# Kernel tuning notes

Measured on AMD Instinct MI355X. Metric: run time of the kernel, lower is better.

The kernel has to match this reference:

```python
import jax, jax.numpy as jnp
import numpy as np


def setup_inputs() -> dict:
    key = jax.random.key(0)
    k1, k2 = jax.random.split(key)
    N, S, C, H, W = 8, 6, 4, 512, 512
    preds = jax.random.normal(k1, (N, S, C, H, W), dtype=jnp.float32)
    targets = jax.random.randint(k2, (N, S, H, W), 0, C, dtype=jnp.int64)
    return {"preds": preds, "targets": targets}


def reference(preds, targets):
    # preds: [N, S, C, H, W], targets: [N, S, H, W]
    # Original: per (target_idx, lat, lon) F.cross_entropy (mean over batch),
    # summed over all pixels and target indices.
    logp = jax.nn.log_softmax(preds, axis=2)              # [N, S, C, H, W]
    tgt = targets[:, :, None, :, :]                        # [N, S, 1, H, W]
    nll = -jnp.take_along_axis(logp, tgt, axis=2)[:, :, 0]  # [N, S, H, W]
    # mean over batch N per pixel, then sum over S, H, W
    return jnp.sum(jnp.mean(nll, axis=0))
```

## Files before the change

### kernel.cpp

```cpp
#include <hip/hip_runtime.h>


#define HW        (512 * 512)
#define QUADS     (HW / 4)
#define NS        48
#define NBLK      ((NS * QUADS) / 256)
#define INV_N     0.125f

typedef float vf4 __attribute__((ext_vector_type(4)));
typedef int   vi4 __attribute__((ext_vector_type(4)));

__device__ __forceinline__ float nll_one(float a, float b, float c, float d, int t) {
    float m = fmaxf(fmaxf(a, b), fmaxf(c, d));
    float s = __expf(a - m) + __expf(b - m) + __expf(c - m) + __expf(d - m);
    float lse = m + __logf(s);
    float xt = (t == 0) ? a : ((t == 1) ? b : ((t == 2) ? c : d));
    return lse - xt;
}

__global__ __launch_bounds__(256) void ce_partial(const float* __restrict__ preds,
                                                  const int* __restrict__ targets,
                                                  float* __restrict__ part) {
    const int g  = blockIdx.x * 256 + threadIdx.x;
    const int ns = g >> 16;
    const int q  = g & (QUADS - 1);

    const vf4* __restrict__ p4 = (const vf4*)preds;
    const vi4* __restrict__ t4 = (const vi4*)targets;

    const int base = (ns << 2) * QUADS + q;
    vf4 x0 = __builtin_nontemporal_load(p4 + base);
    vf4 x1 = __builtin_nontemporal_load(p4 + base + QUADS);
    vf4 x2 = __builtin_nontemporal_load(p4 + base + 2 * QUADS);
    vf4 x3 = __builtin_nontemporal_load(p4 + base + 3 * QUADS);
    vi4 t  = __builtin_nontemporal_load(t4 + ns * QUADS + q);

    float lsum = nll_one(x0.x, x1.x, x2.x, x3.x, t.x)
               + nll_one(x0.y, x1.y, x2.y, x3.y, t.y)
               + nll_one(x0.z, x1.z, x2.z, x3.z, t.z)
               + nll_one(x0.w, x1.w, x2.w, x3.w, t.w);

    #pragma unroll
    for (int off = 32; off > 0; off >>= 1)
        lsum += __shfl_down(lsum, off, 64);

    __shared__ float wsum[4];
    const int lane = threadIdx.x & 63;
    const int wave = threadIdx.x >> 6;
    if (lane == 0) wsum[wave] = lsum;
    __syncthreads();
    if (threadIdx.x == 0)
        part[blockIdx.x] = (wsum[0] + wsum[1] + wsum[2] + wsum[3]) * INV_N;
}

__global__ __launch_bounds__(256) void ce_final(const float* __restrict__ part,
                                                float* __restrict__ out) {
    float lsum = 0.0f;
    #pragma unroll
    for (int i = 0; i < NBLK / 256; ++i)
        lsum += part[i * 256 + threadIdx.x];

    #pragma unroll
    for (int off = 32; off > 0; off >>= 1)
        lsum += __shfl_down(lsum, off, 64);

    __shared__ float wsum[4];
    const int lane = threadIdx.x & 63;
    const int wave = threadIdx.x >> 6;
    if (lane == 0) wsum[wave] = lsum;
    __syncthreads();
    if (threadIdx.x == 0)
        out[0] = wsum[0] + wsum[1] + wsum[2] + wsum[3];
}

extern "C" void kernel_launch(void* const* d_in, const int* in_sizes, int n_in,
                              void* d_out, int out_size, void* d_ws, size_t ws_size,
                              hipStream_t stream) {
    const float* preds   = (const float*)d_in[0];
    const int*   targets = (const int*)d_in[1];
    float*       part    = (float*)d_ws;
    float*       out     = (float*)d_out;

    ce_partial<<<NBLK, 256, 0, stream>>>(preds, targets, part);
    ce_final<<<1, 256, 0, stream>>>(part, out);
}
```

Before: 280.1 us.

## Use persistent grid-stride blocks with double-buffered register prefetch

Replaces the one-quad-per-thread launch (12288 blocks) with 2048 blocks where each thread handles six quads, striding by 8 slices. Loads for the next quad are issued before computing the current one, so two sets of 80 bytes are in flight per thread. This cuts block launch and partial-sum overhead and shrinks the final reduction, at the cost of more registers and fewer resident waves hiding latency.

New measurement: 374.4 us. +33.7%, slower.

```diff
diff --git a/kernel.cpp b/kernel.cpp
--- a/kernel.cpp
+++ b/kernel.cpp
@@ -1,11 +1,17 @@
 #include <hip/hip_runtime.h>
 
 
-#define HW        (512 * 512)
-#define QUADS     (HW / 4)
-#define NS        48
-#define NBLK      ((NS * QUADS) / 256)
-#define INV_N     0.125f
+#define HW      (512 * 512)
+#define QUADS   (HW / 4)
+#define NS      48
+#define NQUAD   (NS * QUADS)
+#define TPB     256
+#define PBLK    2048
+#define STRIDE  (PBLK * TPB)
+#define ITERS   (NQUAD / STRIDE)
+#define PADV    (8 * 4 * QUADS)
+#define TADV    (8 * QUADS)
+#define INV_N   0.125f
 
 typedef float vf4 __attribute__((ext_vector_type(4)));
 typedef int   vi4 __attribute__((ext_vector_type(4)));
@@ -18,27 +24,55 @@
     return lse - xt;
 }
 
-__global__ __launch_bounds__(256) void ce_partial(const float* __restrict__ preds,
-                                                  const int* __restrict__ targets,
-                                                  float* __restrict__ part) {
-    const int g  = blockIdx.x * 256 + threadIdx.x;
-    const int ns = g >> 16;
-    const int q  = g & (QUADS - 1);
+__device__ __forceinline__ float quad_nll(vf4 x0, vf4 x1, vf4 x2, vf4 x3, vi4 t) {
+    return nll_one(x0.x, x1.x, x2.x, x3.x, t.x)
+         + nll_one(x0.y, x1.y, x2.y, x3.y, t.y)
+         + nll_one(x0.z, x1.z, x2.z, x3.z, t.z)
+         + nll_one(x0.w, x1.w, x2.w, x3.w, t.w);
+}
 
-    const vf4* __restrict__ p4 = (const vf4*)preds;
-    const vi4* __restrict__ t4 = (const vi4*)targets;
+__global__ __launch_bounds__(TPB, 8) void ce_partial(const float* __restrict__ preds,
+                                                     const int* __restrict__ targets,
+                                                     float* __restrict__ part) {
+    const int g0  = blockIdx.x * TPB + threadIdx.x;
+    const int ns0 = g0 >> 16;
+    const int q   = g0 & (QUADS - 1);
 
-    const int base = (ns << 2) * QUADS + q;
-    vf4 x0 = __builtin_nontemporal_load(p4 + base);
-    vf4 x1 = __builtin_nontemporal_load(p4 + base + QUADS);
-    vf4 x2 = __builtin_nontemporal_load(p4 + base + 2 * QUADS);
-    vf4 x3 = __builtin_nontemporal_load(p4 + base + 3 * QUADS);
-    vi4 t  = __builtin_nontemporal_load(t4 + ns * QUADS + q);
+    const vf4* __restrict__ p4 = (const vf4*)preds + (size_t)ns0 * (4 * QUADS) + q;
+    const vi4* __restrict__ t4 = (const vi4*)targets + (size_t)ns0 * QUADS + q;
 
-    float lsum = nll_one(x0.x, x1.x, x2.x, x3.x, t.x)
-               + nll_one(x0.y, x1.y, x2.y, x3.y, t.y)
-               + nll_one(x0.z, x1.z, x2.z, x3.z, t.z)
-               + nll_one(x0.w, x1.w, x2.w, x3.w, t.w);
+    vf4 a0 = __builtin_nontemporal_load(p4 + 0 * QUADS);
+    vf4 a1 = __builtin_nontemporal_load(p4 + 1 * QUADS);
+    vf4 a2 = __builtin_nontemporal_load(p4 + 2 * QUADS);
+    vf4 a3 = __builtin_nontemporal_load(p4 + 3 * QUADS);
+    vi4 at = __builtin_nontemporal_load(t4);
+
+    float lsum = 0.0f;
+
+    #pragma unroll
+    for (int i = 0; i < ITERS; i += 2) {
+        const vf4* pb = p4 + (size_t)(i + 1) * PADV;
+        const vi4* tb = t4 + (size_t)(i + 1) * TADV;
+        vf4 b0 = __builtin_nontemporal_load(pb + 0 * QUADS);
+        vf4 b1 = __builtin_nontemporal_load(pb + 1 * QUADS);
+        vf4 b2 = __builtin_nontemporal_load(pb + 2 * QUADS);
+        vf4 b3 = __builtin_nontemporal_load(pb + 3 * QUADS);
+        vi4 bt = __builtin_nontemporal_load(tb);
+
+        lsum += quad_nll(a0, a1, a2, a3, at);
+
+        if (i + 2 < ITERS) {
+            const vf4* pa = p4 + (size_t)(i + 2) * PADV;
+            const vi4* ta = t4 + (size_t)(i + 2) * TADV;
+            a0 = __builtin_nontemporal_load(pa + 0 * QUADS);
+            a1 = __builtin_nontemporal_load(pa + 1 * QUADS);
+            a2 = __builtin_nontemporal_load(pa + 2 * QUADS);
+            a3 = __builtin_nontemporal_load(pa + 3 * QUADS);
+            at = __builtin_nontemporal_load(ta);
+        }
+
+        lsum += quad_nll(b0, b1, b2, b3, bt);
+    }
 
     #pragma unroll
     for (int off = 32; off > 0; off >>= 1)
@@ -57,7 +91,7 @@
                                                 float* __restrict__ out) {
     float lsum = 0.0f;
     #pragma unroll
-    for (int i = 0; i < NBLK / 256; ++i)
+    for (int i = 0; i < PBLK / 256; ++i)
         lsum += part[i * 256 + threadIdx.x];
 
     #pragma unroll
@@ -81,6 +115,6 @@
     float*       part    = (float*)d_ws;
     float*       out     = (float*)d_out;
 
-    ce_partial<<<NBLK, 256, 0, stream>>>(preds, targets, part);
+    ce_partial<<<PBLK, TPB, 0, stream>>>(preds, targets, part);
     ce_final<<<1, 256, 0, stream>>>(part, out);
 }
```

## Use persistent blocks with double-buffered async global-to-LDS loads

Applied to the files above, without the earlier changes.

Replaces the one-quad-per-thread grid with 1024 blocks that loop over the data. Each iteration prefetches the next tile straight into a double-buffered LDS region using global_load_lds and computes on the current tile. The aim is to overlap memory traffic with compute and to cut block-launch and partial-sum overhead. In exchange it adds two block barriers per iteration and LDS round trips, and it keeps fewer independent loads in flight per CU.

New measurement: 306.4 us. 1.09x slower.

```diff
diff --git a/kernel.cpp b/kernel.cpp
--- a/kernel.cpp
+++ b/kernel.cpp
@@ -1,11 +1,16 @@
 #include <hip/hip_runtime.h>
 
 
-#define HW        (512 * 512)
-#define QUADS     (HW / 4)
-#define NS        48
-#define NBLK      ((NS * QUADS) / 256)
-#define INV_N     0.125f
+#define HW      (512 * 512)
+#define QUADS   (HW / 4)
+#define NS      48
+#define NQUAD   (NS * QUADS)
+#define TPB     256
+#define PBLK    1024
+#define ITERS   (NQUAD / (PBLK * TPB))
+#define INV_N   0.125f
+
+#define BUF_FLOATS 5120
 
 typedef float vf4 __attribute__((ext_vector_type(4)));
 typedef int   vi4 __attribute__((ext_vector_type(4)));
@@ -18,38 +23,72 @@
     return lse - xt;
 }
 
-__global__ __launch_bounds__(256) void ce_partial(const float* __restrict__ preds,
+__device__ __forceinline__ float quad_nll(vf4 x0, vf4 x1, vf4 x2, vf4 x3, vi4 t) {
+    return nll_one(x0.x, x1.x, x2.x, x3.x, t.x)
+         + nll_one(x0.y, x1.y, x2.y, x3.y, t.y)
+         + nll_one(x0.z, x1.z, x2.z, x3.z, t.z)
+         + nll_one(x0.w, x1.w, x2.w, x3.w, t.w);
+}
+
+static __device__ __forceinline__ void gld16(const void* g, void* l) {
+    __builtin_amdgcn_global_load_lds(
+        (const __attribute__((address_space(1))) unsigned int*)g,
+        (__attribute__((address_space(3))) unsigned int*)l,
+        16, 0, 0);
+}
+
+__global__ __launch_bounds__(TPB) void ce_partial(const float* __restrict__ preds,
                                                   const int* __restrict__ targets,
                                                   float* __restrict__ part) {
-    const int g  = blockIdx.x * 256 + threadIdx.x;
-    const int ns = g >> 16;
-    const int q  = g & (QUADS - 1);
+    __shared__ float S[2 * BUF_FLOATS];
+
+    const int t    = threadIdx.x;
+    const int lane = t & 63;
+    const int wave = t >> 6;
 
     const vf4* __restrict__ p4 = (const vf4*)preds;
     const vi4* __restrict__ t4 = (const vi4*)targets;
 
-    const int base = (ns << 2) * QUADS + q;
-    vf4 x0 = __builtin_nontemporal_load(p4 + base);
-    vf4 x1 = __builtin_nontemporal_load(p4 + base + QUADS);
-    vf4 x2 = __builtin_nontemporal_load(p4 + base + 2 * QUADS);
-    vf4 x3 = __builtin_nontemporal_load(p4 + base + 3 * QUADS);
-    vi4 t  = __builtin_nontemporal_load(t4 + ns * QUADS + q);
+    float lsum = 0.0f;
 
-    float lsum = nll_one(x0.x, x1.x, x2.x, x3.x, t.x)
-               + nll_one(x0.y, x1.y, x2.y, x3.y, t.y)
-               + nll_one(x0.z, x1.z, x2.z, x3.z, t.z)
-               + nll_one(x0.w, x1.w, x2.w, x3.w, t.w);
+    auto stage = [&](int bb, int it) {
+        const int g0 = (it * PBLK + (int)blockIdx.x) * TPB;
+        const int ns = g0 >> 16;
+        const int q0 = g0 & (QUADS - 1);
+        const int qq = q0 + wave * 64 + lane;
+        float* dst = &S[bb * BUF_FLOATS + wave * 256];
+        #pragma unroll
+        for (int c = 0; c < 4; ++c)
+            gld16(p4 + (size_t)(ns * 4 + c) * QUADS + qq, dst + c * 1024);
+        gld16(t4 + (size_t)ns * QUADS + qq, dst + 4096);
+    };
+
+    stage(0, 0);
+
+    for (int it = 0; it < ITERS; ++it) {
+        const int bb = it & 1;
+        if (it + 1 < ITERS) stage(bb ^ 1, it + 1);
+        __syncthreads();
+
+        const float* B = &S[bb * BUF_FLOATS];
+        vf4 x0 = ((const vf4*)(B))[t];
+        vf4 x1 = ((const vf4*)(B + 1024))[t];
+        vf4 x2 = ((const vf4*)(B + 2048))[t];
+        vf4 x3 = ((const vf4*)(B + 3072))[t];
+        vi4 tt = ((const vi4*)(B + 4096))[t];
+        lsum += quad_nll(x0, x1, x2, x3, tt);
+
+        __syncthreads();
+    }
 
     #pragma unroll
     for (int off = 32; off > 0; off >>= 1)
         lsum += __shfl_down(lsum, off, 64);
 
     __shared__ float wsum[4];
-    const int lane = threadIdx.x & 63;
-    const int wave = threadIdx.x >> 6;
     if (lane == 0) wsum[wave] = lsum;
     __syncthreads();
-    if (threadIdx.x == 0)
+    if (t == 0)
         part[blockIdx.x] = (wsum[0] + wsum[1] + wsum[2] + wsum[3]) * INV_N;
 }
 
@@ -57,7 +96,7 @@
                                                 float* __restrict__ out) {
     float lsum = 0.0f;
     #pragma unroll
-    for (int i = 0; i < NBLK / 256; ++i)
+    for (int i = 0; i < PBLK / 256; ++i)
         lsum += part[i * 256 + threadIdx.x];
 
     #pragma unroll
@@ -81,6 +120,6 @@
     float*       part    = (float*)d_ws;
     float*       out     = (float*)d_out;
 
-    ce_partial<<<NBLK, 256, 0, stream>>>(preds, targets, part);
+    ce_partial<<<PBLK, TPB, 0, stream>>>(preds, targets, part);
     ce_final<<<1, 256, 0, stream>>>(part, out);
 }
```
